# Kernel tuning notes

Measured on AMD Instinct MI355X. Metric: run time of the kernel, lower is better.

The kernel has to match this reference:

```python
import jax, jax.numpy as jnp
import numpy as np

N_HEADS = 16
HEAD_DIM = 128
ROPE_BASE = 10000.0


def _apply_rope(x, start_pos):
    # x: [B, T, H, Dh]; interleaved-pair RoPE (llama-style)
    B, T, H, Dh = x.shape
    half = Dh // 2
    inv_freq = 1.0 / (ROPE_BASE ** (jnp.arange(0, Dh, 2, dtype=jnp.float32) / Dh))  # [half]
    pos = jnp.arange(T, dtype=jnp.float32) + start_pos                              # [T]
    ang = pos[:, None] * inv_freq[None, :]                                          # [T, half]
    cos = jnp.cos(ang)[None, :, None, :].astype(x.dtype)                            # [1,T,1,half]
    sin = jnp.sin(ang)[None, :, None, :].astype(x.dtype)
    x1 = x[..., 0::2]
    x2 = x[..., 1::2]
    r1 = x1 * cos - x2 * sin
    r2 = x1 * sin + x2 * cos
    return jnp.stack([r1, r2], axis=-1).reshape(B, T, H, Dh)


def setup_inputs() -> dict:
    key = jax.random.key(0)
    k0, k1, k2, k3, k4 = jax.random.split(key, 5)
    B, T, D = 2, 2048, 2048
    d_lat = 1024
    x = jax.random.normal(k0, (B, T, D), dtype=jnp.float32)
    wq = jax.random.normal(k1, (D, N_HEADS * HEAD_DIM), dtype=jnp.float32) / np.sqrt(D)
    w_down = jax.random.normal(k2, (D, d_lat), dtype=jnp.float32) / np.sqrt(D)
    w_up = jax.random.normal(k3, (d_lat, 2 * N_HEADS * HEAD_DIM), dtype=jnp.float32) / np.sqrt(d_lat)
    wo = jax.random.normal(k4, (N_HEADS * HEAD_DIM, D), dtype=jnp.float32) / np.sqrt(N_HEADS * HEAD_DIM)
    return {"x": x, "wq": wq, "w_down": w_down, "w_up": w_up, "wo": wo}


def reference(x, wq, w_down, w_up, wo):
    # Prefill path: use_cache=False, mask=None -> causal, start_pos=0, n_kv_heads==n_heads
    B, T, D = x.shape
    H, Dh = N_HEADS, HEAD_DIM
    scale = Dh ** -0.5

    q = (x @ wq).reshape(B, T, H, Dh)
    c_kv = x @ w_down                               # [B, T, d_latent]
    kv_up = (c_kv @ w_up).reshape(B, T, H, 2 * Dh)  # latent decompression
    k, v = kv_up[..., :Dh], kv_up[..., Dh:]

    q = _apply_rope(q, 0)
    k = _apply_rope(k, 0)

    scores = jnp.einsum('bqhd,bkhd->bhqk', q, k) * scale  # [B,H,T,T]
    causal = jnp.tril(jnp.ones((T, T), dtype=bool))
    scores = jnp.where(causal[None, None, :, :], scores, jnp.float32(-jnp.inf))
    attn = jax.nn.softmax(scores, axis=-1)
    out = jnp.einsum('bhqk,bkhd->bqhd', attn, v).reshape(B, T, H * Dh)
    return out @ wo
```

## Files before the change

kernel.cpp:

```cpp
#include <hip/hip_runtime.h>
#include <math.h>
#include <stdint.h>

#define T_SEQ 2048
#define DMODEL 2048
#define DLAT 1024
#define NH 16
#define DH 128
#define BATCH 2
#define MTOT (BATCH * T_SEQ)

typedef float f32x4 __attribute__((ext_vector_type(4)));
typedef __bf16 bf16x8 __attribute__((ext_vector_type(8)));

__device__ __forceinline__ unsigned short f2bf(float f) {
    return __builtin_bit_cast(unsigned short, (__bf16)f);
}

#define EXP2F(x) __builtin_amdgcn_exp2f(x)

__device__ __forceinline__ float red16_max(float v) {
    int x = __builtin_bit_cast(int, v);
    v = fmaxf(v, __builtin_bit_cast(float, __builtin_amdgcn_update_dpp(x, x, 0xB1, 0xf, 0xf, false)));
    x = __builtin_bit_cast(int, v);
    v = fmaxf(v, __builtin_bit_cast(float, __builtin_amdgcn_update_dpp(x, x, 0x4E, 0xf, 0xf, false)));
    x = __builtin_bit_cast(int, v);
    v = fmaxf(v, __builtin_bit_cast(float, __builtin_amdgcn_update_dpp(x, x, 0x124, 0xf, 0xf, false)));
    x = __builtin_bit_cast(int, v);
    v = fmaxf(v, __builtin_bit_cast(float, __builtin_amdgcn_update_dpp(x, x, 0x128, 0xf, 0xf, false)));
    return v;
}
__device__ __forceinline__ float red16_sum(float v) {
    int x = __builtin_bit_cast(int, v);
    v += __builtin_bit_cast(float, __builtin_amdgcn_update_dpp(x, x, 0xB1, 0xf, 0xf, false));
    x = __builtin_bit_cast(int, v);
    v += __builtin_bit_cast(float, __builtin_amdgcn_update_dpp(x, x, 0x4E, 0xf, 0xf, false));
    x = __builtin_bit_cast(int, v);
    v += __builtin_bit_cast(float, __builtin_amdgcn_update_dpp(x, x, 0x124, 0xf, 0xf, false));
    x = __builtin_bit_cast(int, v);
    v += __builtin_bit_cast(float, __builtin_amdgcn_update_dpp(x, x, 0x128, 0xf, 0xf, false));
    return v;
}

#define GLL16(g, l) __builtin_amdgcn_global_load_lds( \
    (const __attribute__((address_space(1))) unsigned int*)(g), \
    (__attribute__((address_space(3))) unsigned int*)(l), 16, 0, 0)

__global__ void rope_table_kernel(float* __restrict__ cosb, float* __restrict__ sinb) {
    int idx = blockIdx.x * blockDim.x + threadIdx.x;
    if (idx >= T_SEQ * 64) return;
    int t = idx >> 6;
    int i = idx & 63;
    float inv = expf(-((2.0f * (float)i) / 128.0f) * logf(10000.0f));
    float ang = (float)t * inv;
    cosb[idx] = cosf(ang);
    sinb[idx] = sinf(ang);
}

__global__ void conv_f2b_kernel(const float* __restrict__ s, unsigned short* __restrict__ d) {
    int i = (blockIdx.x * blockDim.x + threadIdx.x) * 4;
    float4 v = *(const float4*)(s + i);
    ushort4 o;
    o.x = f2bf(v.x); o.y = f2bf(v.y); o.z = f2bf(v.z); o.w = f2bf(v.w);
    *(ushort4*)(d + i) = o;
}

__global__ __launch_bounds__(256)
void transpose_all_kernel(const float* __restrict__ wq, const float* __restrict__ wdn,
                          const float* __restrict__ wup, const float* __restrict__ wo,
                          unsigned short* __restrict__ wqT, unsigned short* __restrict__ wdT,
                          unsigned short* __restrict__ wuT, unsigned short* __restrict__ woT) {
    const int tile = blockIdx.x;
    const float* src; unsigned short* dst; int R, C, local;
    if (tile < 4096)       { src = wq;  dst = wqT; R = 2048; C = 2048; local = tile; }
    else if (tile < 6144)  { src = wdn; dst = wdT; R = 2048; C = 1024; local = tile - 4096; }
    else if (tile < 10240) { src = wup; dst = wuT; R = 1024; C = 4096; local = tile - 6144; }
    else                   { src = wo;  dst = woT; R = 2048; C = 2048; local = tile - 10240; }
    const int ctiles = C >> 5;
    const int c0 = (local & (ctiles - 1)) * 32;
    const int r0 = (local / ctiles) * 32;
    __shared__ unsigned short t16[32][33];
    const int tx = threadIdx.x & 31, ty = threadIdx.x >> 5;
#pragma unroll
    for (int i = 0; i < 32; i += 8)
        t16[ty + i][tx] = f2bf(src[(size_t)(r0 + ty + i) * C + c0 + tx]);
    __syncthreads();
#pragma unroll
    for (int i = 0; i < 32; i += 8)
        dst[(size_t)(c0 + ty + i) * R + r0 + tx] = t16[tx][ty + i];
}

__global__ void transpose_b2b_kernel(const unsigned short* __restrict__ src, unsigned short* __restrict__ dst,
                                     int R, int C) {
    __shared__ unsigned short tile[32][33];
    int tx = threadIdx.x & 31, ty = threadIdx.x >> 5;
    int r0 = blockIdx.y * 32, c0 = blockIdx.x * 32;
#pragma unroll
    for (int i = 0; i < 32; i += 8)
        tile[ty + i][tx] = src[(size_t)(r0 + ty + i) * C + c0 + tx];
    __syncthreads();
#pragma unroll
    for (int i = 0; i < 32; i += 8)
        dst[(size_t)(c0 + ty + i) * R + r0 + tx] = tile[tx][ty + i];
}

template <int EPI>
__global__ __launch_bounds__(512, 2)
void gemm8p_kernel(const unsigned short* __restrict__ A, const unsigned short* __restrict__ BT,
                   void* __restrict__ C0, void* __restrict__ C1,
                   const float* __restrict__ cosb, const float* __restrict__ sinb,
                   int M, int N, int K) {
    __shared__ __align__(16) unsigned short As3[3][128 * 32];
    __shared__ __align__(16) unsigned short Bs3[3][256 * 32];

    const int t = threadIdx.x;
    const int w = t >> 6, l = t & 63;
    const int wr = w >> 2, wc = w & 3;
    const int lr = l & 15, lg = l >> 4;
    const int m0 = blockIdx.y * 128, n0 = blockIdx.x * 256;

    f32x4 acc[4][4] = {{}};
    const int nt = K >> 5;

    auto stage = [&](int kt, int buf) {
        const int k0 = kt << 5;
        {
            int c = t;
            int cc = c ^ (((c >> 5) & 1) << 1);
            GLL16(A + (size_t)(m0 + (c >> 2)) * K + k0 + (cc & 3) * 8, &As3[buf][c * 8]);
        }
#pragma unroll
        for (int u = 0; u < 2; ++u) {
            int c = t + u * 512;
            int cc = c ^ (((c >> 5) & 1) << 1);
            GLL16(BT + (size_t)(n0 + (c >> 2)) * K + k0 + (cc & 3) * 8, &Bs3[buf][c * 8]);
        }
    };

    stage(0, 0);
    stage(1, 1);
    asm volatile("s_waitcnt vmcnt(3)" ::: "memory");
    __builtin_amdgcn_sched_barrier(0);
    __builtin_amdgcn_s_barrier();
    __builtin_amdgcn_sched_barrier(0);

    int cur = 0;
    for (int kt = 0; kt < nt; ++kt) {
        const bool more = (kt + 2) < nt;
        if (more) {
            int nb = cur + 2; if (nb >= 3) nb -= 3;
            stage(kt + 2, nb);
        }
        bf16x8 af[4], bfr[4];
#pragma unroll
        for (int j = 0; j < 4; ++j) {
            int r = wc * 64 + j * 16 + lr;
            int c = (r << 2) + lg; c ^= (((c >> 5) & 1) << 1);
            bfr[j] = *(const bf16x8*)&Bs3[cur][c * 8];
        }
#pragma unroll
        for (int i = 0; i < 4; ++i) {
            int r = wr * 64 + i * 16 + lr;
            int c = (r << 2) + lg; c ^= (((c >> 5) & 1) << 1);
            af[i] = *(const bf16x8*)&As3[cur][c * 8];
        }
        __builtin_amdgcn_s_setprio(1);
#pragma unroll
        for (int i = 0; i < 4; ++i)
#pragma unroll
            for (int j = 0; j < 4; ++j)
                acc[i][j] = __builtin_amdgcn_mfma_f32_16x16x32_bf16(af[i], bfr[j], acc[i][j], 0, 0, 0);
        __builtin_amdgcn_s_setprio(0);
        __builtin_amdgcn_sched_barrier(0);
        if (more) asm volatile("s_waitcnt vmcnt(3)" ::: "memory");
        else      asm volatile("s_waitcnt vmcnt(0)" ::: "memory");
        __builtin_amdgcn_sched_barrier(0);
        __builtin_amdgcn_s_barrier();
        __builtin_amdgcn_sched_barrier(0);
        ++cur; if (cur == 3) cur = 0;
    }

    const float SC2 = 0.08838834764831845f * 1.44269504089f;
    const bool is_cv = (EPI == 4) && (n0 >= 2048);
    const bool is_v2 = (EPI == 2) && (wc >= 2);
#pragma unroll
    for (int i = 0; i < 4; ++i) {
#pragma unroll
        for (int j = 0; j < 4; ++j) {
#pragma unroll
            for (int rr = 0; rr < 4; ++rr) {
                const int row_g = m0 + wr * 64 + i * 16 + lg * 4 + rr;
                const int col_g = n0 + wc * 64 + j * 16 + lr;
                float v = acc[i][j][rr];
                if (EPI == 2) {
                    float res = v;
                    const int d = col_g & 127;
                    if (!is_v2) {
                        float o_ = __shfl_xor(v, 1);
                        int tp = row_g & (T_SEQ - 1);
                        float c = cosb[tp * 64 + (d >> 1)];
                        float s = sinb[tp * 64 + (d >> 1)];
                        res = (lr & 1) ? (o_ * s + v * c) : (v * c - o_ * s);
                    }
                    const int dcol = ((col_g >> 8) << 7) | d;
                    unsigned short* dst = is_v2 ? (unsigned short*)C1 : (unsigned short*)C0;
                    dst[(size_t)row_g * DMODEL + dcol] = f2bf(res);
                } else if (EPI == 3) {
                    ((float*)C0)[(size_t)row_g * N + col_g] = v;
                } else {
                    if (!is_cv) {
                        float o_ = __shfl_xor(v, 1);
                        int d = col_g & 127;
                        int tp = row_g & (T_SEQ - 1);
                        float c = cosb[tp * 64 + (d >> 1)];
                        float s = sinb[tp * 64 + (d >> 1)];
                        float res = (lr & 1) ? (o_ * s + v * c) : (v * c - o_ * s);
                        ((unsigned short*)C0)[(size_t)row_g * DMODEL + col_g] = f2bf(res * SC2);
                    } else {
                        ((unsigned short*)C1)[(size_t)row_g * DLAT + (col_g - 2048)] = f2bf(v);
                    }
                }
            }
        }
    }
}

__global__ __launch_bounds__(256, 2)
void attn_mfma2_kernel(const unsigned short* __restrict__ qb, const unsigned short* __restrict__ kb,
                       const unsigned short* __restrict__ vT, unsigned short* __restrict__ ob) {
    __shared__ __align__(16) unsigned short Ks[64 * 128];
    __shared__ __align__(16) unsigned short Vs[128 * 64];
    __shared__ __align__(16) unsigned short Ps[4][16][64];

    const int bh = blockIdx.x;
    const int b = bh >> 4, h = bh & 15;
    const int qt = 15 - blockIdx.y;
    const int t = threadIdx.x;
    const int w = t >> 6, l = t & 63;
    const int lr = l & 15, lg = l >> 4;

    const unsigned short* kbase = kb + (size_t)(b * T_SEQ) * DMODEL + h * DH;
    const unsigned short* vbase = vT + (size_t)(h * DH) * MTOT + (size_t)b * T_SEQ;

    const int q0 = qt * 128;
    const int q_base = q0 + w * 32;

    bf16x8 qf[2][4];
#pragma unroll
    for (int rg = 0; rg < 2; ++rg) {
        const unsigned short* qrow = qb + (size_t)(b * T_SEQ + q_base + rg * 16 + lr) * DMODEL + h * DH;
#pragma unroll
        for (int c = 0; c < 4; ++c) qf[rg][c] = *(const bf16x8*)(qrow + c * 32 + lg * 8);
    }

    f32x4 o[2][8] = {{}};
    float m[2][4], lsum[2][4];
#pragma unroll
    for (int rg = 0; rg < 2; ++rg)
#pragma unroll
        for (int r = 0; r < 4; ++r) { m[rg][r] = -3.0e38f; lsum[rg][r] = 0.f; }

    const int nt = 2 * qt + 2;

    for (int kt = 0; kt < nt; ++kt) {
        const int k0 = kt * 64;
        __syncthreads();
#pragma unroll
        for (int i = 0; i < 4; ++i) {
            int c = i * 256 + t;
            int row = c >> 4;
            int k16 = (c & 15) ^ (row & 7);
            GLL16(kbase + (size_t)(k0 + row) * DMODEL + k16 * 8, &Ks[c * 8]);
        }
#pragma unroll
        for (int i = 0; i < 4; ++i) {
            int c = i * 256 + t;
            int d = c >> 3;
            int k8 = (c & 7) ^ (d & 7);
            GLL16(vbase + (size_t)d * MTOT + k0 + k8 * 8, &Vs[c * 8]);
        }
        __syncthreads();

        f32x4 s[2][4] = {{}};
        __builtin_amdgcn_s_setprio(1);
#pragma unroll
        for (int j = 0; j < 4; ++j) {
            const int krow = j * 16 + lr;
#pragma unroll
            for (int c = 0; c < 4; ++c) {
                bf16x8 kf = *(const bf16x8*)&Ks[krow * 128 + (((c * 4 + lg) ^ (krow & 7)) * 8)];
                s[0][j] = __builtin_amdgcn_mfma_f32_16x16x32_bf16(qf[0][c], kf, s[0][j], 0, 0, 0);
                s[1][j] = __builtin_amdgcn_mfma_f32_16x16x32_bf16(qf[1][c], kf, s[1][j], 0, 0, 0);
            }
        }
        __builtin_amdgcn_s_setprio(0);

#pragma unroll
        for (int rg = 0; rg < 2; ++rg) {
            const int qb0 = q_base + rg * 16;
            if (k0 + 63 > qb0) {
#pragma unroll
                for (int j = 0; j < 4; ++j) {
                    const int key = k0 + j * 16 + lr;
#pragma unroll
                    for (int r = 0; r < 4; ++r)
                        if (key > qb0 + lg * 4 + r) s[rg][j][r] = -3.0e38f;
                }
            }
            float tm[4];
            int need = 0;
#pragma unroll
            for (int r = 0; r < 4; ++r) {
                float v = fmaxf(fmaxf(s[rg][0][r], s[rg][1][r]), fmaxf(s[rg][2][r], s[rg][3][r]));
                tm[r] = red16_max(v);
                need |= (tm[r] - m[rg][r] > 8.0f) ? 1 : 0;
            }
            if (__any(need)) {
#pragma unroll
                for (int r = 0; r < 4; ++r) {
                    const float mn = fmaxf(m[rg][r], tm[r]);
                    const float a = EXP2F(m[rg][r] - mn);
                    m[rg][r] = mn;
                    lsum[rg][r] *= a;
#pragma unroll
                    for (int i = 0; i < 8; ++i) o[rg][i][r] *= a;
                }
            }
#pragma unroll
            for (int r = 0; r < 4; ++r) {
                float rs = 0.f;
#pragma unroll
                for (int j = 0; j < 4; ++j) { s[rg][j][r] = EXP2F(s[rg][j][r] - m[rg][r]); rs += s[rg][j][r]; }
                lsum[rg][r] += red16_sum(rs);
            }
        }

        bf16x8 pa[2][2];
#pragma unroll
        for (int rg = 0; rg < 2; ++rg) {
#pragma unroll
            for (int j = 0; j < 4; ++j) {
#pragma unroll
                for (int r = 0; r < 4; ++r) {
                    const int prow = lg * 4 + r;
                    const int chunk = (j * 2 + (lr >> 3)) ^ (prow & 7);
                    Ps[w][prow][chunk * 8 + (lr & 7)] = f2bf(s[rg][j][r]);
                }
            }
#pragma unroll
            for (int kc = 0; kc < 2; ++kc)
                pa[rg][kc] = *(const bf16x8*)&Ps[w][lr][((kc * 4 + lg) ^ (lr & 7)) * 8];
        }

        __builtin_amdgcn_s_setprio(1);
#pragma unroll
        for (int i = 0; i < 8; ++i) {
            const int d = i * 16 + lr;
#pragma unroll
            for (int kc = 0; kc < 2; ++kc) {
                bf16x8 vf = *(const bf16x8*)&Vs[d * 64 + (((kc * 4 + lg) ^ (d & 7)) * 8)];
                o[0][i] = __builtin_amdgcn_mfma_f32_16x16x32_bf16(pa[0][kc], vf, o[0][i], 0, 0, 0);
                o[1][i] = __builtin_amdgcn_mfma_f32_16x16x32_bf16(pa[1][kc], vf, o[1][i], 0, 0, 0);
            }
        }
        __builtin_amdgcn_s_setprio(0);
    }

#pragma unroll
    for (int rg = 0; rg < 2; ++rg) {
        float inv[4];
#pragma unroll
        for (int r = 0; r < 4; ++r) inv[r] = 1.f / lsum[rg][r];
#pragma unroll
        for (int i = 0; i < 8; ++i)
#pragma unroll
            for (int r = 0; r < 4; ++r)
                ob[(size_t)(b * T_SEQ + q_base + rg * 16 + lg * 4 + r) * DMODEL + h * DH + i * 16 + lr]
                    = f2bf(o[rg][i][r] * inv[r]);
    }
}

extern "C" void kernel_launch(void* const* d_in, const int* in_sizes, int n_in,
                              void* d_out, int out_size, void* d_ws, size_t ws_size,
                              hipStream_t stream) {
    const float* x      = (const float*)d_in[0];
    const float* wq     = (const float*)d_in[1];
    const float* w_down = (const float*)d_in[2];
    const float* w_up   = (const float*)d_in[3];
    const float* wo     = (const float*)d_in[4];
    float* out = (float*)d_out;

    uint8_t* p = (uint8_t*)d_ws;
    float* cosb = (float*)p;            p += (size_t)T_SEQ * 64 * 4;
    float* sinb = (float*)p;            p += (size_t)T_SEQ * 64 * 4;
    unsigned short* xb   = (unsigned short*)p; p += (size_t)MTOT * DMODEL * 2;
    unsigned short* wqT  = (unsigned short*)p; p += (size_t)DMODEL * DMODEL * 2;
    unsigned short* wdT  = (unsigned short*)p; p += (size_t)DLAT * DMODEL * 2;
    unsigned short* wuT  = (unsigned short*)p; p += (size_t)(2 * NH * DH) * DLAT * 2;
    unsigned short* woT  = (unsigned short*)p; p += (size_t)DMODEL * DMODEL * 2;
    unsigned short* qbuf = (unsigned short*)p; p += (size_t)MTOT * DMODEL * 2;
    unsigned short* ckv  = (unsigned short*)p; p += (size_t)MTOT * DLAT * 2;
    unsigned short* kbuf = (unsigned short*)p; p += (size_t)MTOT * DMODEL * 2;
    unsigned short* vbuf = (unsigned short*)p; p += (size_t)MTOT * DMODEL * 2;
    unsigned short* vT   = (unsigned short*)p; p += (size_t)DMODEL * MTOT * 2;
    unsigned short* abuf = xb;

    rope_table_kernel<<<(T_SEQ * 64) / 256, 256, 0, stream>>>(cosb, sinb);
    conv_f2b_kernel<<<(MTOT * DMODEL / 4) / 256, 256, 0, stream>>>(x, xb);
    transpose_all_kernel<<<14336, 256, 0, stream>>>(wq, w_down, w_up, wo, wqT, wdT, wuT, woT);

    gemm8p_kernel<4><<<dim3((DMODEL + DLAT) / 256, MTOT / 128), 512, 0, stream>>>(
        xb, wqT, qbuf, ckv, cosb, sinb, MTOT, DMODEL + DLAT, DMODEL);
    gemm8p_kernel<2><<<dim3((2 * NH * DH) / 256, MTOT / 128), 512, 0, stream>>>(
        ckv, wuT, kbuf, vbuf, cosb, sinb, MTOT, 2 * NH * DH, DLAT);
    transpose_b2b_kernel<<<dim3(DMODEL / 32, MTOT / 32), 256, 0, stream>>>(vbuf, vT, MTOT, DMODEL);
    attn_mfma2_kernel<<<dim3(BATCH * NH, 16), 256, 0, stream>>>(qbuf, kbuf, vT, abuf);
    gemm8p_kernel<3><<<dim3(DMODEL / 256, MTOT / 128), 512, 0, stream>>>(
        abuf, woT, out, nullptr, cosb, sinb, MTOT, DMODEL, DMODEL);
}
```

Before: 425.7 us.

## Deepen GEMM K-tile to 64 with XCD-swizzled blocks; halve attention query tile

The GEMM now stages 64-wide K tiles (LDS triple buffer grows to 144KB), splits the next-tile prefetch across two MFMA sub-steps, and remaps block IDs so consecutive blocks are spread across the 8 XCDs. The attention kernel shrinks each block to 64 queries with 16 rows per wave, doubling grid size and halving per-wave register state. The aim is fewer barriers per FLOP in the GEMMs and better occupancy and load balance in attention. In exchange, the larger LDS footprint may limit GEMM occupancy, and attention reloads K/V twice as often.

```diff
diff --git a/kernel.cpp b/kernel.cpp
--- a/kernel.cpp
+++ b/kernel.cpp
@@ -106,77 +106,98 @@
 
 template <int EPI>
 __global__ __launch_bounds__(512, 2)
-void gemm8p_kernel(const unsigned short* __restrict__ A, const unsigned short* __restrict__ BT,
+void gemm3p_kernel(const unsigned short* __restrict__ A, const unsigned short* __restrict__ BT,
                    void* __restrict__ C0, void* __restrict__ C1,
                    const float* __restrict__ cosb, const float* __restrict__ sinb,
                    int M, int N, int K) {
-    __shared__ __align__(16) unsigned short As3[3][128 * 32];
-    __shared__ __align__(16) unsigned short Bs3[3][256 * 32];
+    __shared__ __align__(16) unsigned short AL[3][128 * 64];
+    __shared__ __align__(16) unsigned short BL[3][256 * 64];
 
     const int t = threadIdx.x;
     const int w = t >> 6, l = t & 63;
     const int wr = w >> 2, wc = w & 3;
     const int lr = l & 15, lg = l >> 4;
-    const int m0 = blockIdx.y * 128, n0 = blockIdx.x * 256;
+
+    const int gx = gridDim.x;
+    const int nwg = gx * gridDim.y;
+    const int bid = blockIdx.y * gx + blockIdx.x;
+    const int sid = (bid & 7) * (nwg >> 3) + (bid >> 3);
+    const int m0 = (sid / gx) * 128;
+    const int n0 = (sid % gx) * 256;
 
     f32x4 acc[4][4] = {{}};
-    const int nt = K >> 5;
-
-    auto stage = [&](int kt, int buf) {
-        const int k0 = kt << 5;
-        {
-            int c = t;
-            int cc = c ^ (((c >> 5) & 1) << 1);
-            GLL16(A + (size_t)(m0 + (c >> 2)) * K + k0 + (cc & 3) * 8, &As3[buf][c * 8]);
-        }
+    const int nt = K >> 6;
+
+    auto stageA = [&](int kt, int buf) {
+        const int k0 = kt << 6;
 #pragma unroll
         for (int u = 0; u < 2; ++u) {
-            int c = t + u * 512;
-            int cc = c ^ (((c >> 5) & 1) << 1);
-            GLL16(BT + (size_t)(n0 + (c >> 2)) * K + k0 + (cc & 3) * 8, &Bs3[buf][c * 8]);
+            int c = t + (u << 9);
+            int row = c >> 3;
+            int cc = (c & 7) ^ (((row >> 2) & 1) << 1);
+            GLL16(A + (size_t)(m0 + row) * K + k0 + cc * 8, &AL[buf][c * 8]);
         }
     };
-
-    stage(0, 0);
-    stage(1, 1);
-    asm volatile("s_waitcnt vmcnt(3)" ::: "memory");
+    auto stageB = [&](int kt, int buf, int half) {
+        const int k0 = kt << 6;
+#pragma unroll
+        for (int u = 0; u < 2; ++u) {
+            int c = t + (u << 9);
+            int row = c >> 3;
+            int cc = (c & 7) ^ (((row >> 2) & 1) << 1);
+            GLL16(BT + (size_t)(n0 + half * 128 + row) * K + k0 + cc * 8,
+                  &BL[buf][(half * 1024 + c) * 8]);
+        }
+    };
+
+    stageA(0, 0); stageB(0, 0, 0); stageB(0, 0, 1);
+    stageA(1, 1); stageB(1, 1, 0); stageB(1, 1, 1);
+    asm volatile("s_waitcnt vmcnt(6)" ::: "memory");
     __builtin_amdgcn_sched_barrier(0);
     __builtin_amdgcn_s_barrier();
-    __builtin_amdgcn_sched_barrier(0);
 
     int cur = 0;
     for (int kt = 0; kt < nt; ++kt) {
         const bool more = (kt + 2) < nt;
-        if (more) {
-            int nb = cur + 2; if (nb >= 3) nb -= 3;
-            stage(kt + 2, nb);
-        }
-        bf16x8 af[4], bfr[4];
-#pragma unroll
-        for (int j = 0; j < 4; ++j) {
-            int r = wc * 64 + j * 16 + lr;
-            int c = (r << 2) + lg; c ^= (((c >> 5) & 1) << 1);
-            bfr[j] = *(const bf16x8*)&Bs3[cur][c * 8];
-        }
-#pragma unroll
-        for (int i = 0; i < 4; ++i) {
-            int r = wr * 64 + i * 16 + lr;
-            int c = (r << 2) + lg; c ^= (((c >> 5) & 1) << 1);
-            af[i] = *(const bf16x8*)&As3[cur][c * 8];
-        }
-        __builtin_amdgcn_s_setprio(1);
-#pragma unroll
-        for (int i = 0; i < 4; ++i)
-#pragma unroll
-            for (int j = 0; j < 4; ++j)
-                acc[i][j] = __builtin_amdgcn_mfma_f32_16x16x32_bf16(af[i], bfr[j], acc[i][j], 0, 0, 0);
-        __builtin_amdgcn_s_setprio(0);
-        __builtin_amdgcn_sched_barrier(0);
-        if (more) asm volatile("s_waitcnt vmcnt(3)" ::: "memory");
-        else      asm volatile("s_waitcnt vmcnt(0)" ::: "memory");
-        __builtin_amdgcn_sched_barrier(0);
-        __builtin_amdgcn_s_barrier();
-        __builtin_amdgcn_sched_barrier(0);
+        int nb = cur + 2; if (nb >= 3) nb -= 3;
+
+#pragma unroll
+        for (int kk = 0; kk < 2; ++kk) {
+            bf16x8 af[4], bfr[4];
+#pragma unroll
+            for (int i = 0; i < 4; ++i) {
+                int row = wr * 64 + i * 16 + lr;
+                int ch = (kk * 4 + lg) ^ (((row >> 2) & 1) << 1);
+                af[i] = *(const bf16x8*)&AL[cur][(row * 8 + ch) * 8];
+            }
+#pragma unroll
+            for (int j = 0; j < 4; ++j) {
+                int row = wc * 64 + j * 16 + lr;
+                int ch = (kk * 4 + lg) ^ (((row >> 2) & 1) << 1);
+                bfr[j] = *(const bf16x8*)&BL[cur][(row * 8 + ch) * 8];
+            }
+            if (more) {
+                if (kk == 0) { stageA(kt + 2, nb); stageB(kt + 2, nb, 0); }
+                else         { stageB(kt + 2, nb, 1); }
+            }
+            __builtin_amdgcn_s_barrier();
+            __builtin_amdgcn_s_setprio(1);
+#pragma unroll
+            for (int i = 0; i < 4; ++i)
+#pragma unroll
+                for (int j = 0; j < 4; ++j)
+                    acc[i][j] = __builtin_amdgcn_mfma_f32_16x16x32_bf16(af[i], bfr[j], acc[i][j], 0, 0, 0);
+            __builtin_amdgcn_s_setprio(0);
+            if (kk == 0) {
+                __builtin_amdgcn_s_barrier();
+            } else {
+                __builtin_amdgcn_sched_barrier(0);
+                if (more) asm volatile("s_waitcnt vmcnt(6)" ::: "memory");
+                else      asm volatile("s_waitcnt vmcnt(0)" ::: "memory");
+                __builtin_amdgcn_sched_barrier(0);
+                __builtin_amdgcn_s_barrier();
+            }
+        }
         ++cur; if (cur == 3) cur = 0;
     }
 
@@ -226,7 +247,7 @@
 }
 
 __global__ __launch_bounds__(256, 2)
-void attn_mfma2_kernel(const unsigned short* __restrict__ qb, const unsigned short* __restrict__ kb,
+void attn_mfma3_kernel(const unsigned short* __restrict__ qb, const unsigned short* __restrict__ kb,
                        const unsigned short* __restrict__ vT, unsigned short* __restrict__ ob) {
     __shared__ __align__(16) unsigned short Ks[64 * 128];
     __shared__ __align__(16) unsigned short Vs[128 * 64];
@@ -234,7 +255,7 @@
 
     const int bh = blockIdx.x;
     const int b = bh >> 4, h = bh & 15;
-    const int qt = 15 - blockIdx.y;
+    const int qt = 31 - blockIdx.y;
     const int t = threadIdx.x;
     const int w = t >> 6, l = t & 63;
     const int lr = l & 15, lg = l >> 4;
@@ -242,25 +263,21 @@
     const unsigned short* kbase = kb + (size_t)(b * T_SEQ) * DMODEL + h * DH;
     const unsigned short* vbase = vT + (size_t)(h * DH) * MTOT + (size_t)b * T_SEQ;
 
-    const int q0 = qt * 128;
-    const int q_base = q0 + w * 32;
-
-    bf16x8 qf[2][4];
-#pragma unroll
-    for (int rg = 0; rg < 2; ++rg) {
-        const unsigned short* qrow = qb + (size_t)(b * T_SEQ + q_base + rg * 16 + lr) * DMODEL + h * DH;
-#pragma unroll
-        for (int c = 0; c < 4; ++c) qf[rg][c] = *(const bf16x8*)(qrow + c * 32 + lg * 8);
+    const int q_base = qt * 64 + w * 16;
+
+    bf16x8 qf[4];
+    {
+        const unsigned short* qrow = qb + (size_t)(b * T_SEQ + q_base + lr) * DMODEL + h * DH;
+#pragma unroll
+        for (int c = 0; c < 4; ++c) qf[c] = *(const bf16x8*)(qrow + c * 32 + lg * 8);
     }
 
-    f32x4 o[2][8] = {{}};
-    float m[2][4], lsum[2][4];
-#pragma unroll
-    for (int rg = 0; rg < 2; ++rg)
-#pragma unroll
-        for (int r = 0; r < 4; ++r) { m[rg][r] = -3.0e38f; lsum[rg][r] = 0.f; }
-
-    const int nt = 2 * qt + 2;
+    f32x4 o[8] = {};
+    float m[4], lsum[4];
+#pragma unroll
+    for (int r = 0; r < 4; ++r) { m[r] = -3.0e38f; lsum[r] = 0.f; }
+
+    const int nt = qt + 1;
 
     for (int kt = 0; kt < nt; ++kt) {
         const int k0 = kt * 64;
@@ -281,7 +298,7 @@
         }
         __syncthreads();
 
-        f32x4 s[2][4] = {{}};
+        f32x4 s[4] = {};
         __builtin_amdgcn_s_setprio(1);
 #pragma unroll
         for (int j = 0; j < 4; ++j) {
@@ -289,68 +306,60 @@
 #pragma unroll
             for (int c = 0; c < 4; ++c) {
                 bf16x8 kf = *(const bf16x8*)&Ks[krow * 128 + (((c * 4 + lg) ^ (krow & 7)) * 8)];
-                s[0][j] = __builtin_amdgcn_mfma_f32_16x16x32_bf16(qf[0][c], kf, s[0][j], 0, 0, 0);
-                s[1][j] = __builtin_amdgcn_mfma_f32_16x16x32_bf16(qf[1][c], kf, s[1][j], 0, 0, 0);
+                s[j] = __builtin_amdgcn_mfma_f32_16x16x32_bf16(qf[c], kf, s[j], 0, 0, 0);
             }
         }
         __builtin_amdgcn_s_setprio(0);
 
-#pragma unroll
-        for (int rg = 0; rg < 2; ++rg) {
-            const int qb0 = q_base + rg * 16;
-            if (k0 + 63 > qb0) {
-#pragma unroll
-                for (int j = 0; j < 4; ++j) {
-                    const int key = k0 + j * 16 + lr;
-#pragma unroll
-                    for (int r = 0; r < 4; ++r)
-                        if (key > qb0 + lg * 4 + r) s[rg][j][r] = -3.0e38f;
-                }
-            }
-            float tm[4];
-            int need = 0;
+        if (k0 + 63 > q_base) {
+#pragma unroll
+            for (int j = 0; j < 4; ++j) {
+                const int key = k0 + j * 16 + lr;
+#pragma unroll
+                for (int r = 0; r < 4; ++r)
+                    if (key > q_base + lg * 4 + r) s[j][r] = -3.0e38f;
+            }
+        }
+        float tm[4];
+        int need = 0;
+#pragma unroll
+        for (int r = 0; r < 4; ++r) {
+            float v = fmaxf(fmaxf(s[0][r], s[1][r]), fmaxf(s[2][r], s[3][r]));
+            tm[r] = red16_max(v);
+            need |= (tm[r] - m[r] > 8.0f) ? 1 : 0;
+        }
+        if (__any(need)) {
 #pragma unroll
             for (int r = 0; r < 4; ++r) {
-                float v = fmaxf(fmaxf(s[rg][0][r], s[rg][1][r]), fmaxf(s[rg][2][r], s[rg][3][r]));
-                tm[r] = red16_max(v);
-                need |= (tm[r] - m[rg][r] > 8.0f) ? 1 : 0;
-            }
-            if (__any(need)) {
-#pragma unroll
-                for (int r = 0; r < 4; ++r) {
-                    const float mn = fmaxf(m[rg][r], tm[r]);
-                    const float a = EXP2F(m[rg][r] - mn);
-                    m[rg][r] = mn;
-                    lsum[rg][r] *= a;
-#pragma unroll
-                    for (int i = 0; i < 8; ++i) o[rg][i][r] *= a;
-                }
-            }
+                const float mn = fmaxf(m[r], tm[r]);
+                const float a = EXP2F(m[r] - mn);
+                m[r] = mn;
+                lsum[r] *= a;
+#pragma unroll
+                for (int i = 0; i < 8; ++i) o[i][r] *= a;
+            }
+        }
+#pragma unroll
+        for (int r = 0; r < 4; ++r) {
+            float rs = 0.f;
+#pragma unroll
+            for (int j = 0; j < 4; ++j) { s[j][r] = EXP2F(s[j][r] - m[r]); rs += s[j][r]; }
+            lsum[r] += red16_sum(rs);
+        }
+
+        bf16x8 pa[2];
+#pragma unroll
+        for (int j = 0; j < 4; ++j) {
 #pragma unroll
             for (int r = 0; r < 4; ++r) {
-                float rs = 0.f;
-#pragma unroll
-                for (int j = 0; j < 4; ++j) { s[rg][j][r] = EXP2F(s[rg][j][r] - m[rg][r]); rs += s[rg][j][r]; }
-                lsum[rg][r] += red16_sum(rs);
-            }
-        }
-
-        bf16x8 pa[2][2];
-#pragma unroll
-        for (int rg = 0; rg < 2; ++rg) {
-#pragma unroll
-            for (int j = 0; j < 4; ++j) {
-#pragma unroll
-                for (int r = 0; r < 4; ++r) {
-                    const int prow = lg * 4 + r;
-                    const int chunk = (j * 2 + (lr >> 3)) ^ (prow & 7);
-                    Ps[w][prow][chunk * 8 + (lr & 7)] = f2bf(s[rg][j][r]);
-                }
-            }
-#pragma unroll
-            for (int kc = 0; kc < 2; ++kc)
-                pa[rg][kc] = *(const bf16x8*)&Ps[w][lr][((kc * 4 + lg) ^ (lr & 7)) * 8];
-        }
+                const int prow = lg * 4 + r;
+                const int chunk = (j * 2 + (lr >> 3)) ^ (prow & 7);
+                Ps[w][prow][chunk * 8 + (lr & 7)] = f2bf(s[j][r]);
+            }
+        }
+#pragma unroll
+        for (int kc = 0; kc < 2; ++kc)
+            pa[kc] = *(const bf16x8*)&Ps[w][lr][((kc * 4 + lg) ^ (lr & 7)) * 8];
 
         __builtin_amdgcn_s_setprio(1);
 #pragma unroll
@@ -359,25 +368,21 @@
 #pragma unroll
             for (int kc = 0; kc < 2; ++kc) {
                 bf16x8 vf = *(const bf16x8*)&Vs[d * 64 + (((kc * 4 + lg) ^ (d & 7)) * 8)];
-                o[0][i] = __builtin_amdgcn_mfma_f32_16x16x32_bf16(pa[0][kc], vf, o[0][i], 0, 0, 0);
-                o[1][i] = __builtin_amdgcn_mfma_f32_16x16x32_bf16(pa[1][kc], vf, o[1][i], 0, 0, 0);
+                o[i] = __builtin_amdgcn_mfma_f32_16x16x32_bf16(pa[kc], vf, o[i], 0, 0, 0);
             }
         }
         __builtin_amdgcn_s_setprio(0);
     }
 
-#pragma unroll
-    for (int rg = 0; rg < 2; ++rg) {
-        float inv[4];
-#pragma unroll
-        for (int r = 0; r < 4; ++r) inv[r] = 1.f / lsum[rg][r];
-#pragma unroll
-        for (int i = 0; i < 8; ++i)
-#pragma unroll
-            for (int r = 0; r < 4; ++r)
-                ob[(size_t)(b * T_SEQ + q_base + rg * 16 + lg * 4 + r) * DMODEL + h * DH + i * 16 + lr]
-                    = f2bf(o[rg][i][r] * inv[r]);
-    }
+    float inv[4];
+#pragma unroll
+    for (int r = 0; r < 4; ++r) inv[r] = 1.f / lsum[r];
+#pragma unroll
+    for (int i = 0; i < 8; ++i)
+#pragma unroll
+        for (int r = 0; r < 4; ++r)
+            ob[(size_t)(b * T_SEQ + q_base + lg * 4 + r) * DMODEL + h * DH + i * 16 + lr]
+                = f2bf(o[i][r] * inv[r]);
 }
 
 extern "C" void kernel_launch(void* const* d_in, const int* in_sizes, int n_in,
@@ -409,12 +414,12 @@
     conv_f2b_kernel<<<(MTOT * DMODEL / 4) / 256, 256, 0, stream>>>(x, xb);
     transpose_all_kernel<<<14336, 256, 0, stream>>>(wq, w_down, w_up, wo, wqT, wdT, wuT, woT);
 
-    gemm8p_kernel<4><<<dim3((DMODEL + DLAT) / 256, MTOT / 128), 512, 0, stream>>>(
+    gemm3p_kernel<4><<<dim3((DMODEL + DLAT) / 256, MTOT / 128), 512, 0, stream>>>(
         xb, wqT, qbuf, ckv, cosb, sinb, MTOT, DMODEL + DLAT, DMODEL);
-    gemm8p_kernel<2><<<dim3((2 * NH * DH) / 256, MTOT / 128), 512, 0, stream>>>(
+    gemm3p_kernel<2><<<dim3((2 * NH * DH) / 256, MTOT / 128), 512, 0, stream>>>(
         ckv, wuT, kbuf, vbuf, cosb, sinb, MTOT, 2 * NH * DH, DLAT);
     transpose_b2b_kernel<<<dim3(DMODEL / 32, MTOT / 32), 256, 0, stream>>>(vbuf, vT, MTOT, DMODEL);
-    attn_mfma2_kernel<<<dim3(BATCH * NH, 16), 256, 0, stream>>>(qbuf, kbuf, vT, abuf);
-    gemm8p_kernel<3><<<dim3(DMODEL / 256, MTOT / 128), 512, 0, stream>>>(
+    attn_mfma3_kernel<<<dim3(BATCH * NH, 32), 256, 0, stream>>>(qbuf, kbuf, vT, abuf);
+    gemm3p_kernel<3><<<dim3(DMODEL / 256, MTOT / 128), 512, 0, stream>>>(
         abuf, woT, out, nullptr, cosb, sinb, MTOT, DMODEL, DMODEL);
 }
```

Result: faster. 415.4 us (-2.4%).
